# Kernel tuning notes

Hardware: AMD Instinct MI355X
Metric: run time of the kernel (lower is better)

## Reference

```python
import jax, jax.numpy as jnp
import numpy as np

N_NODES = 50000
N_EDGES = 400000
D_IN = 2048
D_OUT = 512


def setup_inputs() -> dict:
    key = jax.random.key(0)
    k1, k2, k3 = jax.random.split(key, 3)
    x = jax.random.normal(k1, (N_NODES, D_IN), dtype=jnp.float32)
    edge_index = jax.random.randint(k2, (2, N_EDGES), 0, N_NODES, dtype=jnp.int64)
    # Glorot init like PyG GCNConv
    scale = jnp.sqrt(6.0 / (D_IN + D_OUT)).astype(jnp.float32)
    weight = jax.random.uniform(k3, (D_IN, D_OUT), dtype=jnp.float32, minval=-scale, maxval=scale)
    bias = jnp.zeros((D_OUT,), dtype=jnp.float32)
    return {"x": x, "edge_index": edge_index, "weight": weight, "bias": bias}


def reference(x, edge_index, weight, bias):
    N = x.shape[0]
    # GCNConv(normalize=True): add self-loops, symmetric deg^-1/2 normalization
    loops = jnp.arange(N, dtype=edge_index.dtype)
    src = jnp.concatenate([edge_index[0], loops])  # message sources (x_j)
    dst = jnp.concatenate([edge_index[1], loops])  # aggregation targets
    ones = jnp.ones(dst.shape[0], dtype=x.dtype)
    deg = jax.ops.segment_sum(ones, dst, num_segments=N)  # [N]
    deg_inv_sqrt = jnp.where(deg > 0, jax.lax.rsqrt(deg), 0.0)
    norm = deg_inv_sqrt[src] * deg_inv_sqrt[dst]  # [E+N]
    h = x @ weight  # [N, d_out] linear transform before propagation
    msgs = norm[:, None] * h[src]  # [E+N, d_out]
    out = jax.ops.segment_sum(msgs, dst, num_segments=N) + bias  # [N, d_out]
    return jax.nn.log_softmax(out, axis=1)
```

## Files before the change

kernel.cpp:

```cpp
#include <hip/hip_runtime.h>
#include <stdint.h>

#define D_IN   2048
#define D_OUT  512

typedef __bf16 bf16;
typedef bf16     bf16x8 __attribute__((ext_vector_type(8)));
typedef float    f32x4  __attribute__((ext_vector_type(4)));
typedef uint32_t u32x4  __attribute__((ext_vector_type(4)));

#define GLP(p)  (const __attribute__((address_space(1))) void*)(p)
#define LDSP(p) (__attribute__((address_space(3))) void*)(p)

__global__ void k_count(const int* __restrict__ dstv, int* __restrict__ cnt, int E) {
    int e = blockIdx.x * blockDim.x + threadIdx.x;
    if (e < E) atomicAdd(&cnt[dstv[e]], 1);
}

__global__ void k_dis(const int* __restrict__ cnt, float* __restrict__ dis, int n) {
    int i = blockIdx.x * blockDim.x + threadIdx.x;
    if (i < n) dis[i] = rsqrtf((float)(cnt[i] + 1));
}

__global__ __launch_bounds__(1024) void k_scan1(const int* __restrict__ cnt,
                                                int* __restrict__ offs,
                                                int* __restrict__ bsum, int n) {
    __shared__ int wsum[16], wbase[16];
    const int tid = threadIdx.x, lane = tid & 63, wv = tid >> 6;
    int i = blockIdx.x * 1024 + tid;
    int v = (i < n) ? cnt[i] : 0;
    int x = v;
    #pragma unroll
    for (int d = 1; d < 64; d <<= 1) {
        int y = __shfl_up(x, d);
        if (lane >= d) x += y;
    }
    if (lane == 63) wsum[wv] = x;
    __syncthreads();
    if (tid < 16) {
        int s = 0;
        for (int j = 0; j < tid; ++j) s += wsum[j];
        wbase[tid] = s;
    }
    __syncthreads();
    if (i < n) offs[i] = wbase[wv] + x - v;
    if (tid == 0) bsum[blockIdx.x] = wbase[15] + wsum[15];
}

__global__ void k_scan2(int* __restrict__ bsum, int nb) {
    int t = threadIdx.x;
    if (nb <= 64) {
        int v = (t < nb) ? bsum[t] : 0;
        int x = v;
        #pragma unroll
        for (int d = 1; d < 64; d <<= 1) {
            int y = __shfl_up(x, d);
            if (t >= d) x += y;
        }
        if (t < nb) bsum[t] = x - v;
    } else if (t == 0) {
        int run = 0;
        for (int j = 0; j < nb; ++j) { int v = bsum[j]; bsum[j] = run; run += v; }
    }
}

__global__ void k_scan3(int* __restrict__ offs, const int* __restrict__ bsum, int n) {
    int i = blockIdx.x * blockDim.x + threadIdx.x;
    if (i < n) offs[i] += bsum[i >> 10];
}

__global__ void k_fill(const int* __restrict__ srcv, const int* __restrict__ dstv,
                       const int* __restrict__ offs, int* __restrict__ cur,
                       int* __restrict__ csr, int E) {
    int e = blockIdx.x * blockDim.x + threadIdx.x;
    if (e < E) {
        int d = dstv[e];
        int p = offs[d] + atomicAdd(&cur[d], 1);
        csr[p] = srcv[e];
    }
}

__global__ void k_wt(const float* __restrict__ W, uint16_t* __restrict__ wt) {
    __shared__ float t[32][33];
    int kb = blockIdx.x * 32, nb = blockIdx.y * 32;
    int tx = threadIdx.x, ty = threadIdx.y;
    #pragma unroll
    for (int i = 0; i < 32; i += 8)
        t[ty + i][tx] = W[(size_t)(kb + ty + i) * D_OUT + nb + tx];
    __syncthreads();
    bf16* o = (bf16*)wt;
    #pragma unroll
    for (int i = 0; i < 32; i += 8)
        o[(size_t)(nb + ty + i) * D_IN + kb + tx] = (bf16)t[tx][ty + i];
}

__global__ __launch_bounds__(256) void k_gemm(const float* __restrict__ X,
                                              const uint16_t* __restrict__ WT,
                                              uint16_t* __restrict__ H, int M) {
    __shared__ float    lsA[2][128 * 32];
    __shared__ uint16_t lsB[128 * 64];
    const int nwg = gridDim.x;
    const int b = blockIdx.x;
    const int q = nwg >> 3, r = nwg & 7;
    const int xcd = b & 7, lo = b >> 3;
    const int g = (xcd < r) ? (xcd * (q + 1) + lo) : (r * (q + 1) + (xcd - r) * q + lo);
    const int m0 = (g >> 2) * 128;
    const int n0 = (g & 3) * 128;
    const int tid = threadIdx.x;
    const int w = tid >> 6, lane = tid & 63;
    const int wr = w >> 1, wc = w & 1;
    const int lr = lane & 15, lk = lane >> 4;

    f32x4 acc[4][4];
    #pragma unroll
    for (int m = 0; m < 4; m++)
        #pragma unroll
        for (int n = 0; n < 4; n++) acc[m][n] = (f32x4)(0.0f);

    const float* aSrc[2][4];
    const uint16_t* bSrc[4];
    #pragma unroll
    for (int j = 0; j < 4; j++) {
        int c = w * 4 + j;
        int uidx = c * 64 + lane;
        int row = uidx >> 3, u = uidx & 7;
        int lrow = row;
        if (m0 + row >= M) lrow = (M - 1) - m0;
        const float* rbase = X + (size_t)(m0 + lrow) * D_IN;
        #pragma unroll
        for (int h = 0; h < 2; h++)
            aSrc[h][j] = rbase + h * 32 + (u ^ (row & 7)) * 4;
        bSrc[j] = WT + (size_t)(n0 + row) * D_IN + (u ^ (row & 7)) * 8;
    }

    for (int k0 = 0; k0 < D_IN; k0 += 64) {
        #pragma unroll
        for (int h = 0; h < 2; h++)
            #pragma unroll
            for (int j = 0; j < 4; j++)
                __builtin_amdgcn_global_load_lds(GLP(aSrc[h][j] + k0),
                                                 LDSP(lsA[h] + (w * 4 + j) * 256), 16, 0, 0);
        #pragma unroll
        for (int j = 0; j < 4; j++)
            __builtin_amdgcn_global_load_lds(GLP(bSrc[j] + k0),
                                             LDSP(lsB + (w * 4 + j) * 512), 16, 0, 0);
        __syncthreads();

        #pragma unroll
        for (int kk = 0; kk < 2; kk++) {
            bf16x8 aF[4], bF[4];
            #pragma unroll
            for (int m = 0; m < 4; m++) {
                int row = wr * 64 + m * 16 + lr;
                const float* base = lsA[kk] + row * 32;
                f32x4 a0 = *(const f32x4*)(base + (((2 * lk)    ) ^ (row & 7)) * 4);
                f32x4 a1 = *(const f32x4*)(base + (((2 * lk) + 1) ^ (row & 7)) * 4);
                bf16x8 af;
                af[0] = (bf16)a0[0]; af[1] = (bf16)a0[1]; af[2] = (bf16)a0[2]; af[3] = (bf16)a0[3];
                af[4] = (bf16)a1[0]; af[5] = (bf16)a1[1]; af[6] = (bf16)a1[2]; af[7] = (bf16)a1[3];
                aF[m] = af;
            }
            #pragma unroll
            for (int n = 0; n < 4; n++) {
                int row = wc * 64 + n * 16 + lr;
                bF[n] = *(const bf16x8*)((const bf16*)lsB + row * 64 + (((kk * 4 + lk) ^ (row & 7)) * 8));
            }
            #pragma unroll
            for (int m = 0; m < 4; m++)
                #pragma unroll
                for (int n = 0; n < 4; n++)
                    acc[m][n] = __builtin_amdgcn_mfma_f32_16x16x32_bf16(aF[m], bF[n], acc[m][n], 0, 0, 0);
        }
        __syncthreads();
    }

    #pragma unroll
    for (int m = 0; m < 4; m++) {
        int rbase = m0 + wr * 64 + m * 16 + lk * 4;
        #pragma unroll
        for (int n = 0; n < 4; n++) {
            int col = n0 + wc * 64 + n * 16 + lr;
            #pragma unroll
            for (int j = 0; j < 4; j++) {
                int row = rbase + j;
                if (row < M) {
                    bf16 t = (bf16)acc[m][n][j];
                    H[(size_t)row * D_OUT + col] = __builtin_bit_cast(uint16_t, t);
                }
            }
        }
    }
}

__global__ __launch_bounds__(256) void k_agg(const uint16_t* __restrict__ h,
                                             const int* __restrict__ csr,
                                             const int* __restrict__ offs,
                                             const int* __restrict__ cnt,
                                             const float* __restrict__ dis,
                                             const float* __restrict__ bias,
                                             float* __restrict__ out, int N) {
    const int wv = threadIdx.x >> 6, lane = threadIdx.x & 63;
    const int i = blockIdx.x * 4 + wv;
    if (i >= N) return;
    const float di = dis[i];
    float acc[8];
    {
        u32x4 v = *(const u32x4*)(h + (size_t)i * D_OUT + lane * 8);
        float s2 = di * di;
        #pragma unroll
        for (int k = 0; k < 4; k++) {
            acc[2 * k]     = __builtin_bit_cast(float, v[k] << 16) * s2;
            acc[2 * k + 1] = __builtin_bit_cast(float, v[k] & 0xffff0000u) * s2;
        }
    }
    const int o = offs[i], c = cnt[i];
    for (int e = o; e < o + c; ++e) {
        int s = csr[e];
        float ws = di * dis[s];
        u32x4 v = *(const u32x4*)(h + (size_t)s * D_OUT + lane * 8);
        #pragma unroll
        for (int k = 0; k < 4; k++) {
            acc[2 * k]     += __builtin_bit_cast(float, v[k] << 16) * ws;
            acc[2 * k + 1] += __builtin_bit_cast(float, v[k] & 0xffff0000u) * ws;
        }
    }
    {
        const f32x4* bp = (const f32x4*)(bias + lane * 8);
        f32x4 b0 = bp[0], b1 = bp[1];
        #pragma unroll
        for (int k = 0; k < 4; k++) { acc[k] += b0[k]; acc[4 + k] += b1[k]; }
    }
    float mx = acc[0];
    #pragma unroll
    for (int k = 1; k < 8; k++) mx = fmaxf(mx, acc[k]);
    #pragma unroll
    for (int d = 1; d < 64; d <<= 1) mx = fmaxf(mx, __shfl_xor(mx, d));
    float se = 0.f;
    #pragma unroll
    for (int k = 0; k < 8; k++) se += expf(acc[k] - mx);
    #pragma unroll
    for (int d = 1; d < 64; d <<= 1) se += __shfl_xor(se, d);
    float lse = mx + logf(se);
    f32x4 o0, o1;
    #pragma unroll
    for (int k = 0; k < 4; k++) { o0[k] = acc[k] - lse; o1[k] = acc[4 + k] - lse; }
    f32x4* op = (f32x4*)(out + (size_t)i * D_OUT + lane * 8);
    op[0] = o0; op[1] = o1;
}

extern "C" void kernel_launch(void* const* d_in, const int* in_sizes, int n_in,
                              void* d_out, int out_size, void* d_ws, size_t ws_size,
                              hipStream_t stream) {
    const float* x    = (const float*)d_in[0];
    const int*   ei   = (const int*)d_in[1];
    const float* W    = (const float*)d_in[2];
    const float* bias = (const float*)d_in[3];
    float* out = (float*)d_out;

    const int N = in_sizes[0] / D_IN;
    const int E = in_sizes[1] / 2;
    const int* srcv = ei;
    const int* dstv = ei + E;

    char* p = (char*)d_ws;
    auto carve = [&](size_t b) { void* r = (void*)p; p += (b + 255) & ~(size_t)255; return r; };
    uint16_t* h    = (uint16_t*)carve((size_t)N * D_OUT * 2);
    uint16_t* wt   = (uint16_t*)carve((size_t)D_OUT * D_IN * 2);
    int*      cnt  = (int*)carve((size_t)N * 4);
    int*      cur  = (int*)carve((size_t)N * 4);
    float*    dis  = (float*)carve((size_t)N * 4);
    int*      offs = (int*)carve((size_t)N * 4);
    int*      csr  = (int*)carve((size_t)E * 4);
    int*      bsum = (int*)carve(1024 * 4);

    hipMemsetAsync(cnt, 0, ((size_t)N * 4 + 255 & ~(size_t)255) + (size_t)N * 4, stream);

    k_wt<<<dim3(D_IN / 32, D_OUT / 32), dim3(32, 8), 0, stream>>>(W, wt);
    k_count<<<(E + 255) / 256, 256, 0, stream>>>(dstv, cnt, E);
    k_dis<<<(N + 255) / 256, 256, 0, stream>>>(cnt, dis, N);
    const int nb = (N + 1023) / 1024;
    k_scan1<<<nb, 1024, 0, stream>>>(cnt, offs, bsum, N);
    k_scan2<<<1, 64, 0, stream>>>(bsum, nb);
    k_scan3<<<(N + 255) / 256, 256, 0, stream>>>(offs, bsum, N);
    k_fill<<<(E + 255) / 256, 256, 0, stream>>>(srcv, dstv, offs, cur, csr, E);

    k_gemm<<<((N + 127) / 128) * 4, 256, 0, stream>>>(x, wt, h, N);

    k_agg<<<(N + 3) / 4, 256, 0, stream>>>(h, csr, offs, cnt, dis, bias, out, N);
}
```

Measured before the change: 342.6 us.

## Fuse degree/scan kernels, precompute per-edge norms, unroll aggregation loop by two

Folds the rsqrt degree computation and the cur-array reset into the block scan kernel. It drops the scan-add pass by adding the block prefix inside the fill and aggregate kernels. The fill kernel now also writes a per-edge source norm array, so aggregation reads contiguous weights instead of gathering dis[s]. The aggregation loop is unrolled by two to keep two neighbor row loads in flight, at the cost of an extra E-sized buffer and more registers.

Result: faster. 329.3 us (median of 3 runs) (-3.9%).

```diff
diff --git a/kernel.cpp b/kernel.cpp
--- a/kernel.cpp
+++ b/kernel.cpp
@@ -17,14 +17,11 @@
     if (e < E) atomicAdd(&cnt[dstv[e]], 1);
 }
 
-__global__ void k_dis(const int* __restrict__ cnt, float* __restrict__ dis, int n) {
-    int i = blockIdx.x * blockDim.x + threadIdx.x;
-    if (i < n) dis[i] = rsqrtf((float)(cnt[i] + 1));
-}
-
 __global__ __launch_bounds__(1024) void k_scan1(const int* __restrict__ cnt,
                                                 int* __restrict__ offs,
-                                                int* __restrict__ bsum, int n) {
+                                                int* __restrict__ bsum,
+                                                float* __restrict__ dis,
+                                                int* __restrict__ cur, int n) {
     __shared__ int wsum[16], wbase[16];
     const int tid = threadIdx.x, lane = tid & 63, wv = tid >> 6;
     int i = blockIdx.x * 1024 + tid;
@@ -43,7 +40,11 @@
         wbase[tid] = s;
     }
     __syncthreads();
-    if (i < n) offs[i] = wbase[wv] + x - v;
+    if (i < n) {
+        offs[i] = wbase[wv] + x - v;
+        dis[i]  = rsqrtf((float)(v + 1));
+        cur[i]  = 0;
+    }
     if (tid == 0) bsum[blockIdx.x] = wbase[15] + wsum[15];
 }
 
@@ -64,19 +65,17 @@
     }
 }
 
-__global__ void k_scan3(int* __restrict__ offs, const int* __restrict__ bsum, int n) {
-    int i = blockIdx.x * blockDim.x + threadIdx.x;
-    if (i < n) offs[i] += bsum[i >> 10];
-}
-
 __global__ void k_fill(const int* __restrict__ srcv, const int* __restrict__ dstv,
-                       const int* __restrict__ offs, int* __restrict__ cur,
-                       int* __restrict__ csr, int E) {
+                       const int* __restrict__ offs, const int* __restrict__ bsum,
+                       const float* __restrict__ dis, int* __restrict__ cur,
+                       int* __restrict__ csr, float* __restrict__ nrm, int E) {
     int e = blockIdx.x * blockDim.x + threadIdx.x;
     if (e < E) {
         int d = dstv[e];
-        int p = offs[d] + atomicAdd(&cur[d], 1);
-        csr[p] = srcv[e];
+        int s = srcv[e];
+        int p = offs[d] + bsum[d >> 10] + atomicAdd(&cur[d], 1);
+        csr[p] = s;
+        nrm[p] = dis[s];
     }
 }
 
@@ -194,7 +193,9 @@
 
 __global__ __launch_bounds__(256) void k_agg(const uint16_t* __restrict__ h,
                                              const int* __restrict__ csr,
+                                             const float* __restrict__ nrm,
                                              const int* __restrict__ offs,
+                                             const int* __restrict__ bsum,
                                              const int* __restrict__ cnt,
                                              const float* __restrict__ dis,
                                              const float* __restrict__ bias,
@@ -213,15 +214,32 @@
             acc[2 * k + 1] = __builtin_bit_cast(float, v[k] & 0xffff0000u) * s2;
         }
     }
-    const int o = offs[i], c = cnt[i];
-    for (int e = o; e < o + c; ++e) {
-        int s = csr[e];
-        float ws = di * dis[s];
-        u32x4 v = *(const u32x4*)(h + (size_t)s * D_OUT + lane * 8);
+    const int o = offs[i] + bsum[i >> 10], c = cnt[i];
+    int e = o;
+    for (; e + 2 <= o + c; e += 2) {
+        int s0 = csr[e], s1 = csr[e + 1];
+        float w0 = di * nrm[e], w1 = di * nrm[e + 1];
+        u32x4 v0 = *(const u32x4*)(h + (size_t)s0 * D_OUT + lane * 8);
+        u32x4 v1 = *(const u32x4*)(h + (size_t)s1 * D_OUT + lane * 8);
         #pragma unroll
         for (int k = 0; k < 4; k++) {
-            acc[2 * k]     += __builtin_bit_cast(float, v[k] << 16) * ws;
-            acc[2 * k + 1] += __builtin_bit_cast(float, v[k] & 0xffff0000u) * ws;
+            acc[2 * k]     += __builtin_bit_cast(float, v0[k] << 16) * w0;
+            acc[2 * k + 1] += __builtin_bit_cast(float, v0[k] & 0xffff0000u) * w0;
+        }
+        #pragma unroll
+        for (int k = 0; k < 4; k++) {
+            acc[2 * k]     += __builtin_bit_cast(float, v1[k] << 16) * w1;
+            acc[2 * k + 1] += __builtin_bit_cast(float, v1[k] & 0xffff0000u) * w1;
+        }
+    }
+    if (e < o + c) {
+        int s0 = csr[e];
+        float w0 = di * nrm[e];
+        u32x4 v0 = *(const u32x4*)(h + (size_t)s0 * D_OUT + lane * 8);
+        #pragma unroll
+        for (int k = 0; k < 4; k++) {
+            acc[2 * k]     += __builtin_bit_cast(float, v0[k] << 16) * w0;
+            acc[2 * k + 1] += __builtin_bit_cast(float, v0[k] & 0xffff0000u) * w0;
         }
     }
     {
@@ -271,20 +289,19 @@
     float*    dis  = (float*)carve((size_t)N * 4);
     int*      offs = (int*)carve((size_t)N * 4);
     int*      csr  = (int*)carve((size_t)E * 4);
+    float*    nrm  = (float*)carve((size_t)E * 4);
     int*      bsum = (int*)carve(1024 * 4);
 
-    hipMemsetAsync(cnt, 0, ((size_t)N * 4 + 255 & ~(size_t)255) + (size_t)N * 4, stream);
+    hipMemsetAsync(cnt, 0, (size_t)N * 4, stream);
 
     k_wt<<<dim3(D_IN / 32, D_OUT / 32), dim3(32, 8), 0, stream>>>(W, wt);
     k_count<<<(E + 255) / 256, 256, 0, stream>>>(dstv, cnt, E);
-    k_dis<<<(N + 255) / 256, 256, 0, stream>>>(cnt, dis, N);
     const int nb = (N + 1023) / 1024;
-    k_scan1<<<nb, 1024, 0, stream>>>(cnt, offs, bsum, N);
+    k_scan1<<<nb, 1024, 0, stream>>>(cnt, offs, bsum, dis, cur, N);
     k_scan2<<<1, 64, 0, stream>>>(bsum, nb);
-    k_scan3<<<(N + 255) / 256, 256, 0, stream>>>(offs, bsum, N);
-    k_fill<<<(E + 255) / 256, 256, 0, stream>>>(srcv, dstv, offs, cur, csr, E);
+    k_fill<<<(E + 255) / 256, 256, 0, stream>>>(srcv, dstv, offs, bsum, dis, cur, csr, nrm, E);
 
     k_gemm<<<((N + 127) / 128) * 4, 256, 0, stream>>>(x, wt, h, N);
 
-    k_agg<<<(N + 3) / 4, 256, 0, stream>>>(h, csr, offs, cnt, dis, bias, out, N);
-}
+    k_agg<<<(N + 3) / 4, 256, 0, stream>>>(h, csr, nrm, offs, bsum, cnt, dis, bias, out, N);
+}
```
